# Optimization experiments

Measured on AMD Instinct MI355X. Metric: run time of the kernel, lower is better.

## Reference

```python
import jax, jax.numpy as jnp
import numpy as np

HIDDEN = 1024
HEADS = 16
HEAD_DIM = HIDDEN // HEADS          # 64
ROT = 2 * (HEAD_DIM // 3 // 2)      # 20 (d/h/w rotary chunk), residual = 4
GRID = 256 // 16                    # crop_size // patch_size = 16
DEPTH = 16 // 2                     # frames_per_clip // tubelet_size = 8
N_VIDEO = DEPTH * GRID * GRID       # 2048
N_ACTION = 16
B = 2
SCALE = HEAD_DIM ** -0.5


def _rope(x, pos):
    # interleaved RoPE (VJEPA2 rotate_queries_or_keys): pairs (x[2i], x[2i+1])
    D = x.shape[-1]
    omega = 1.0 / (10000.0 ** (jnp.arange(D // 2, dtype=x.dtype) / (D / 2.0)))
    freq = pos.astype(x.dtype)[..., None] * omega          # (N, D/2)
    cos, sin = jnp.cos(freq), jnp.sin(freq)
    x1, x2 = x[..., 0::2], x[..., 1::2]
    return jnp.stack([x1 * cos - x2 * sin, x2 * cos + x1 * sin], axis=-1).reshape(x.shape)


def _rope3(qk, d_pos, h_pos, w_pos):
    # rotate three ROT-sized chunks (depth/height/width axes), leave residual dims as-is
    parts = [_rope(qk[..., 0:ROT], d_pos),
             _rope(qk[..., ROT:2 * ROT], h_pos),
             _rope(qk[..., 2 * ROT:3 * ROT], w_pos)]
    if 3 * ROT < HEAD_DIM:
        parts.append(qk[..., 3 * ROT:])
    return jnp.concatenate(parts, axis=-1)


def _forward(video_hidden_states, action_hidden_states, W_q, b_q, W_k, b_k, W_v, b_v,
             W_qa, b_qa, W_ka, b_ka, W_va, b_va, W_proj, b_proj, W_proj_a, b_proj_a):
    Bsz, Nv, _ = video_hidden_states.shape
    Na = action_hidden_states.shape[1]

    def proj(x, W, b):  # -> (B, H, N, Dh)
        y = x @ W.T + b
        return y.reshape(Bsz, -1, HEADS, HEAD_DIM).transpose(0, 2, 1, 3)

    qv = proj(video_hidden_states, W_q, b_q)
    kv = proj(video_hidden_states, W_k, b_k)
    vv = proj(video_hidden_states, W_v, b_v)

    # 3-axis position ids for raster-ordered video tokens
    ids = jnp.arange(Nv)
    tpf = GRID * GRID
    d_pos = ids // tpf
    rem = ids - tpf * d_pos
    h_pos = rem // GRID
    w_pos = rem - GRID * h_pos

    qv = _rope3(qv, d_pos, h_pos, w_pos)
    kv = _rope3(kv, d_pos, h_pos, w_pos)

    qa = proj(action_hidden_states, W_qa, b_qa)
    ka = proj(action_hidden_states, W_ka, b_ka)
    va = proj(action_hidden_states, W_va, b_va)

    # actions: linspace between frame-id of token 0 and token 1 (faithful to source)
    a_pos = jnp.linspace(d_pos[0].astype(jnp.float32), d_pos[1].astype(jnp.float32), Na)
    qa = _rope3(qa, a_pos, a_pos, a_pos)
    ka = _rope3(ka, a_pos, a_pos, a_pos)

    # joint attention over concatenated video+action token sequence
    q = jnp.concatenate([qv, qa], axis=2)
    k = jnp.concatenate([kv, ka], axis=2)
    v = jnp.concatenate([vv, va], axis=2)

    scores = jnp.einsum('bhqd,bhkd->bhqk', q, k) * SCALE
    probs = jax.nn.softmax(scores, axis=-1)
    ctx = jnp.einsum('bhqk,bhkd->bhqd', probs, v)
    ctx = ctx.transpose(0, 2, 1, 3).reshape(Bsz, Nv + Na, HIDDEN)

    out_video = ctx[:, :Nv] @ W_proj.T + b_proj
    out_action = ctx[:, Nv:] @ W_proj_a.T + b_proj_a
    return out_video, out_action


def setup_inputs() -> dict:
    key = jax.random.key(0)
    ks = jax.random.split(key, 12)
    sd = HIDDEN ** -0.5
    inp = {}
    for i, n in enumerate(['q', 'k', 'v', 'qa', 'ka', 'va', 'proj', 'proj_a']):
        inp[f'W_{n}'] = jax.random.normal(ks[i], (HIDDEN, HIDDEN), jnp.float32) * sd
        inp[f'b_{n}'] = jnp.zeros((HIDDEN,), jnp.float32)
    inp['video_hidden_states'] = jax.random.normal(ks[10], (B, N_VIDEO, HIDDEN), jnp.float32)
    inp['action_hidden_states'] = jax.random.normal(ks[11], (B, N_ACTION, HIDDEN), jnp.float32)
    return inp


def reference(video_hidden_states, action_hidden_states, W_q, b_q, W_k, b_k, W_v, b_v,
              W_qa, b_qa, W_ka, b_ka, W_va, b_va, W_proj, b_proj, W_proj_a, b_proj_a):
    return _forward(video_hidden_states, action_hidden_states, W_q, b_q, W_k, b_k, W_v, b_v,
                    W_qa, b_qa, W_ka, b_ka, W_va, b_va, W_proj, b_proj, W_proj_a, b_proj_a)
```

## Files before the change

kernel.cpp:

```cpp
#include <hip/hip_runtime.h>
#include <stdint.h>

#define HID   1024
#define NHEAD 16
#define HDIM  64
#define NV    2048
#define NA    16
#define NTOK  2064
#define BSZ   2
#define EXP_C1 0.18033688011112042f
#define EXP_C2 16.0f

typedef __bf16 bf16x8 __attribute__((ext_vector_type(8)));
typedef unsigned short u16x8 __attribute__((ext_vector_type(8)));
typedef unsigned short u16x4 __attribute__((ext_vector_type(4)));
typedef float f32x4 __attribute__((ext_vector_type(4)));

__device__ __forceinline__ unsigned short f2bf(float f) {
  unsigned u = __builtin_bit_cast(unsigned, f);
  u += 0x7FFFu + ((u >> 16) & 1u);
  return (unsigned short)(u >> 16);
}
__device__ __forceinline__ unsigned short f2bf_trunc(float f) {
  return (unsigned short)(__builtin_bit_cast(unsigned, f) >> 16);
}

__global__ __launch_bounds__(256) void qkv_kernel(
    const float* __restrict__ video, const float* __restrict__ action,
    const float* __restrict__ Wq, const float* __restrict__ bq,
    const float* __restrict__ Wk, const float* __restrict__ bk,
    const float* __restrict__ Wv, const float* __restrict__ bv,
    const float* __restrict__ Wqa, const float* __restrict__ bqa,
    const float* __restrict__ Wka, const float* __restrict__ bka,
    const float* __restrict__ Wva, const float* __restrict__ bva,
    unsigned short* __restrict__ Qo, unsigned short* __restrict__ Ko,
    unsigned short* __restrict__ Vt)
{
  __shared__ unsigned short As[64][40];
  __shared__ unsigned short Bs[64][40];

  const int tid  = threadIdx.x;
  const int wave = tid >> 6;
  const int lane = tid & 63;
  const int quad = lane >> 4;
  const int l16  = lane & 15;
  const int z    = blockIdx.z;
  const int y    = blockIdx.y;
  const int head = blockIdx.x;
  const int n0   = head * 64;

  int b, rows, tok0; const float* X; bool act;
  if (y < 64) { b = y >> 5; tok0 = (y & 31) * 64; rows = 64;
                X = video + ((size_t)b * NV + tok0) * HID; act = false; }
  else        { b = y - 64; tok0 = NV; rows = NA;
                X = action + (size_t)b * NA * HID; act = true; }

  const float* W; const float* bias; 
  if (z == 0)      { W = act ? Wqa : Wq; bias = act ? bqa : bq; }
  else if (z == 1) { W = act ? Wka : Wk; bias = act ? bka : bk; }
  else             { W = act ? Wva : Wv; bias = act ? bva : bv; }

  const int arow = tid >> 2;
  const int ac8  = (tid & 3) * 8;
  const int xr   = min(arow, rows - 1);

  f32x4 acc[4] = {};

  for (int kt = 0; kt < HID; kt += 32) {
    {
      const float* src = X + (size_t)xr * HID + kt + ac8;
      float4 f0 = *(const float4*)src;
      float4 f1 = *(const float4*)(src + 4);
      u16x8 v;
      v[0]=f2bf(f0.x); v[1]=f2bf(f0.y); v[2]=f2bf(f0.z); v[3]=f2bf(f0.w);
      v[4]=f2bf(f1.x); v[5]=f2bf(f1.y); v[6]=f2bf(f1.z); v[7]=f2bf(f1.w);
      *(u16x8*)&As[arow][ac8] = v;
    }
    {
      const float* src = W + (size_t)(n0 + arow) * HID + kt + ac8;
      float4 f0 = *(const float4*)src;
      float4 f1 = *(const float4*)(src + 4);
      u16x8 v;
      v[0]=f2bf(f0.x); v[1]=f2bf(f0.y); v[2]=f2bf(f0.z); v[3]=f2bf(f0.w);
      v[4]=f2bf(f1.x); v[5]=f2bf(f1.y); v[6]=f2bf(f1.z); v[7]=f2bf(f1.w);
      *(u16x8*)&Bs[arow][ac8] = v;
    }
    __syncthreads();
    bf16x8 a = __builtin_bit_cast(bf16x8, *(const u16x8*)&As[wave * 16 + l16][quad * 8]);
#pragma unroll
    for (int nt = 0; nt < 4; nt++) {
      bf16x8 bb = __builtin_bit_cast(bf16x8, *(const u16x8*)&Bs[nt * 16 + l16][quad * 8]);
      acc[nt] = __builtin_amdgcn_mfma_f32_16x16x32_bf16(a, bb, acc[nt], 0, 0, 0);
    }
    __syncthreads();
  }

  const int mbase = wave * 16 + quad * 4;

  if (z < 2) {
    unsigned short* O = (z == 0) ? Qo : Ko;
#pragma unroll
    for (int nt = 0; nt < 4; nt++) {
      const int col = nt * 16 + l16;
      float vals[4];
#pragma unroll
      for (int r = 0; r < 4; r++) vals[r] = acc[nt][r] + bias[n0 + col];
      if (!act && col < 60) {
        const int seg = (col >= 40) ? 2 : (col >= 20) ? 1 : 0;
        const int tin = col - seg * 20;
        const int jj  = tin >> 1;
        const bool evn = !(tin & 1);
        const float om = exp2f(-(float)jj * 1.3287712379549449f);
#pragma unroll
        for (int r = 0; r < 4; r++) {
          int tk = tok0 + mbase + r;
          int dp = tk >> 8, hp = (tk >> 4) & 15, wp = tk & 15;
          float pos = (seg == 0) ? (float)dp : (seg == 1) ? (float)hp : (float)wp;
          float fr = pos * om;
          float cs = cosf(fr), sn = sinf(fr);
          float part = __shfl_xor(vals[r], 1);
          vals[r] = evn ? (vals[r] * cs - part * sn) : (vals[r] * cs + part * sn);
        }
      }
#pragma unroll
      for (int r = 0; r < 4; r++) {
        int m = mbase + r;
        if (m < rows)
          O[(((size_t)b * NHEAD + head) * NTOK + tok0 + m) * HDIM + col] = f2bf(vals[r]);
      }
    }
  } else {
#pragma unroll
    for (int nt = 0; nt < 4; nt++) {
      const int col = nt * 16 + l16;
      u16x4 pk;
#pragma unroll
      for (int r = 0; r < 4; r++) pk[r] = f2bf(acc[nt][r] + bias[n0 + col]);
      if (mbase < rows)
        *(u16x4*)&Vt[(((size_t)b * NHEAD + head) * HDIM + col) * NTOK + tok0 + mbase] = pk;
    }
  }
}

__global__ __launch_bounds__(256) void attn_kernel(
    const unsigned short* __restrict__ Q,
    const unsigned short* __restrict__ K,
    const unsigned short* __restrict__ Vt,
    unsigned short* __restrict__ ctx)
{
  __shared__ unsigned short Qs[64][72];
  __shared__ unsigned short Ks[64][72];
  __shared__ unsigned short Vts[64][72];
  __shared__ unsigned short Ps[4][16][68];

  const int tid  = threadIdx.x;
  const int wave = tid >> 6;
  const int lane = tid & 63;
  const int quad = lane >> 4;
  const int l16  = lane & 15;
  const int bh   = blockIdx.y;
  const int q0   = blockIdx.x * 64;
  const unsigned short* Qp  = Q  + (size_t)bh * NTOK * HDIM;
  const unsigned short* Kp  = K  + (size_t)bh * NTOK * HDIM;
  const unsigned short* Vtp = Vt + (size_t)bh * HDIM * NTOK;

  const int r  = tid >> 2;
  const int c0 = (tid & 3) * 8;

  {
    int row = min(q0 + r, NTOK - 1);
#pragma unroll
    for (int cc = 0; cc < 2; cc++) {
      int c = c0 + cc * 32;
      *(u16x8*)&Qs[r][c] = *(const u16x8*)(Qp + (size_t)row * HDIM + c);
    }
  }

  u16x8 ones_u;
#pragma unroll
  for (int i = 0; i < 8; i++) ones_u[i] = 0x3F80;
  const bf16x8 ones = __builtin_bit_cast(bf16x8, ones_u);

  f32x4 oacc[4] = {};
  f32x4 lacc = {};

  for (int kv0 = 0; kv0 < NTOK; kv0 += 64) {
    __syncthreads();
    {
      int row = min(kv0 + r, NTOK - 1);
#pragma unroll
      for (int cc = 0; cc < 2; cc++) {
        int c = c0 + cc * 32;
        *(u16x8*)&Ks[r][c]  = *(const u16x8*)(Kp + (size_t)row * HDIM + c);
        *(u16x8*)&Vts[r][c] = *(const u16x8*)(Vtp + (size_t)r * NTOK + kv0 + c);
      }
    }
    __syncthreads();

    f32x4 sacc[4] = {};
#pragma unroll
    for (int kq = 0; kq < 64; kq += 32) {
      bf16x8 a = __builtin_bit_cast(bf16x8, *(const u16x8*)&Qs[wave * 16 + l16][kq + quad * 8]);
#pragma unroll
      for (int nt = 0; nt < 4; nt++) {
        bf16x8 bb = __builtin_bit_cast(bf16x8, *(const u16x8*)&Ks[nt * 16 + l16][kq + quad * 8]);
        sacc[nt] = __builtin_amdgcn_mfma_f32_16x16x32_bf16(a, bb, sacc[nt], 0, 0, 0);
      }
    }

#pragma unroll
    for (int nt = 0; nt < 4; nt++) {
      bool valid = (kv0 + nt * 16 + l16) < NTOK;
#pragma unroll
      for (int rr = 0; rr < 4; rr++) {
        float p = exp2f(__builtin_fmaf(sacc[nt][rr], EXP_C1, -EXP_C2));
        p = valid ? p : 0.f;
        Ps[wave][quad * 4 + rr][nt * 16 + l16] = f2bf_trunc(p);
      }
    }

#pragma unroll
    for (int kq = 0; kq < 64; kq += 32) {
      u16x4 alo = *(const u16x4*)&Ps[wave][l16][kq + quad * 8];
      u16x4 ahi = *(const u16x4*)&Ps[wave][l16][kq + quad * 8 + 4];
      bf16x8 a = __builtin_bit_cast(bf16x8,
          __builtin_shufflevector(alo, ahi, 0, 1, 2, 3, 4, 5, 6, 7));
#pragma unroll
      for (int nt = 0; nt < 4; nt++) {
        bf16x8 bb = __builtin_bit_cast(bf16x8, *(const u16x8*)&Vts[nt * 16 + l16][kq + quad * 8]);
        oacc[nt] = __builtin_amdgcn_mfma_f32_16x16x32_bf16(a, bb, oacc[nt], 0, 0, 0);
      }
      lacc = __builtin_amdgcn_mfma_f32_16x16x32_bf16(a, ones, lacc, 0, 0, 0);
    }
  }

  const int b = bh >> 4, h = bh & 15;
  float rl[4];
#pragma unroll
  for (int rr = 0; rr < 4; rr++) rl[rr] = 1.f / lacc[rr];
#pragma unroll
  for (int nt = 0; nt < 4; nt++) {
#pragma unroll
    for (int rr = 0; rr < 4; rr++) {
      int token = q0 + wave * 16 + quad * 4 + rr;
      if (token < NTOK) {
        int d = nt * 16 + l16;
        ctx[((size_t)b * NTOK + token) * HID + h * HDIM + d] = f2bf(oacc[nt][rr] * rl[rr]);
      }
    }
  }
}

__global__ __launch_bounds__(256) void proj_kernel(
    const unsigned short* __restrict__ ctx,
    const float* __restrict__ Wp, const float* __restrict__ bp,
    const float* __restrict__ Wpa, const float* __restrict__ bpa,
    float* __restrict__ out)
{
  __shared__ unsigned short As[64][40];
  __shared__ unsigned short Bs[64][40];

  const int tid  = threadIdx.x;
  const int wave = tid >> 6;
  const int lane = tid & 63;
  const int quad = lane >> 4;
  const int l16  = lane & 15;
  const int y    = blockIdx.y;
  const int n0   = blockIdx.x * 64;

  int b, rows, tok0; bool act;
  if (y < 64) { b = y >> 5; tok0 = (y & 31) * 64; rows = 64; act = false; }
  else        { b = y - 64; tok0 = NV; rows = NA; act = true; }

  const unsigned short* X = ctx + ((size_t)b * NTOK + tok0) * HID;
  const float* W = act ? Wpa : Wp;
  const float* bias = act ? bpa : bp;

  const int arow = tid >> 2;
  const int ac8  = (tid & 3) * 8;
  const int xr   = min(arow, rows - 1);

  f32x4 acc[4] = {};

  for (int kt = 0; kt < HID; kt += 32) {
    *(u16x8*)&As[arow][ac8] = *(const u16x8*)(X + (size_t)xr * HID + kt + ac8);
    {
      const float* src = W + (size_t)(n0 + arow) * HID + kt + ac8;
      float4 f0 = *(const float4*)src;
      float4 f1 = *(const float4*)(src + 4);
      u16x8 v;
      v[0]=f2bf(f0.x); v[1]=f2bf(f0.y); v[2]=f2bf(f0.z); v[3]=f2bf(f0.w);
      v[4]=f2bf(f1.x); v[5]=f2bf(f1.y); v[6]=f2bf(f1.z); v[7]=f2bf(f1.w);
      *(u16x8*)&Bs[arow][ac8] = v;
    }
    __syncthreads();
    bf16x8 a = __builtin_bit_cast(bf16x8, *(const u16x8*)&As[wave * 16 + l16][quad * 8]);
#pragma unroll
    for (int nt = 0; nt < 4; nt++) {
      bf16x8 bb = __builtin_bit_cast(bf16x8, *(const u16x8*)&Bs[nt * 16 + l16][quad * 8]);
      acc[nt] = __builtin_amdgcn_mfma_f32_16x16x32_bf16(a, bb, acc[nt], 0, 0, 0);
    }
    __syncthreads();
  }

#pragma unroll
  for (int nt = 0; nt < 4; nt++) {
#pragma unroll
    for (int r = 0; r < 4; r++) {
      int m = wave * 16 + quad * 4 + r;
      if (m < rows) {
        int colg = n0 + nt * 16 + l16;
        float val = acc[nt][r] + bias[colg];
        if (!act)
          out[((size_t)b * NV + tok0 + m) * HID + colg] = val;
        else
          out[(size_t)BSZ * NV * HID + ((size_t)b * NA + m) * HID + colg] = val;
      }
    }
  }
}

extern "C" void kernel_launch(void* const* d_in, const int* in_sizes, int n_in,
                              void* d_out, int out_size, void* d_ws, size_t ws_size,
                              hipStream_t stream) {
  const float* A[18];
  if (in_sizes[0] == HID * HID) {
    for (int i = 0; i < 18; i++) A[i] = (const float*)d_in[i];
  } else {
    A[16] = (const float*)d_in[0];
    A[17] = (const float*)d_in[1];
    for (int i = 0; i < 16; i++) A[i] = (const float*)d_in[i + 2];
  }
  const float *Wq = A[0], *bq = A[1], *Wk = A[2], *bk = A[3], *Wv = A[4], *bv = A[5];
  const float *Wqa = A[6], *bqa = A[7], *Wka = A[8], *bka = A[9], *Wva = A[10], *bva = A[11];
  const float *Wp = A[12], *bp = A[13], *Wpa = A[14], *bpa = A[15];
  const float *video = A[16], *action = A[17];
  float* out = (float*)d_out;

  const size_t qkv_elems = (size_t)BSZ * NHEAD * NTOK * HDIM;
  unsigned short* Qw  = (unsigned short*)d_ws;
  unsigned short* Kw  = Qw + qkv_elems;
  unsigned short* Vtw = Kw + qkv_elems;
  unsigned short* ctx = Vtw + qkv_elems;

  dim3 g1(16, 66, 3);
  qkv_kernel<<<g1, 256, 0, stream>>>(video, action, Wq, bq, Wk, bk, Wv, bv,
                                     Wqa, bqa, Wka, bka, Wva, bva, Qw, Kw, Vtw);
  dim3 g3(33, BSZ * NHEAD);
  attn_kernel<<<g3, 256, 0, stream>>>(Qw, Kw, Vtw, ctx);
  dim3 g4(16, 66);
  proj_kernel<<<g4, 256, 0, stream>>>(ctx, Wp, bp, Wpa, bpa, out);
}
```

Baseline: 371.5 us.

## Pre-convert inputs to bf16 and use 128x128 async-LDS GEMM tiles for projections

Adds a conversion kernel that turns all weights and activations into bf16 once, instead of converting fp32 inside every GEMM tile load. The QKV and output projection GEMMs move from 64x64 to 128x128 tiles, with each wave computing a 4x4 grid of MFMA tiles, and load tiles with global_load_lds direct-to-LDS copies. Video and action rows are flattened into one M dimension, which changes the ctx layout. In exchange there is an extra launch plus workspace traffic, the LDS tiles are unpadded so bank conflicts are possible, and the larger tiles yield fewer blocks.

```diff
diff --git a/kernel.cpp b/kernel.cpp
--- a/kernel.cpp
+++ b/kernel.cpp
@@ -8,6 +8,8 @@
 #define NA    16
 #define NTOK  2064
 #define BSZ   2
+#define MROWS 4128
+#define WSZ   1048576
 #define EXP_C1 0.18033688011112042f
 #define EXP_C2 16.0f
 
@@ -24,120 +26,155 @@
 __device__ __forceinline__ unsigned short f2bf_trunc(float f) {
   return (unsigned short)(__builtin_bit_cast(unsigned, f) >> 16);
 }
-
-__global__ __launch_bounds__(256) void qkv_kernel(
+__device__ __forceinline__ void async_copy16(const void* g, void* l) {
+  __builtin_amdgcn_global_load_lds(
+      (const __attribute__((address_space(1))) unsigned int*)g,
+      (__attribute__((address_space(3))) unsigned int*)l, 16, 0, 0);
+}
+
+__global__ __launch_bounds__(256) void cvt_kernel(
+    const float* __restrict__ W0, const float* __restrict__ W1,
+    const float* __restrict__ W2, const float* __restrict__ W3,
+    const float* __restrict__ W4, const float* __restrict__ W5,
+    const float* __restrict__ W6, const float* __restrict__ W7,
     const float* __restrict__ video, const float* __restrict__ action,
-    const float* __restrict__ Wq, const float* __restrict__ bq,
-    const float* __restrict__ Wk, const float* __restrict__ bk,
-    const float* __restrict__ Wv, const float* __restrict__ bv,
-    const float* __restrict__ Wqa, const float* __restrict__ bqa,
-    const float* __restrict__ Wka, const float* __restrict__ bka,
-    const float* __restrict__ Wva, const float* __restrict__ bva,
+    unsigned short* __restrict__ Wb, unsigned short* __restrict__ Xb)
+{
+  const int y = blockIdx.y;
+  const size_t idx = ((size_t)blockIdx.x * 256 + threadIdx.x) * 8;
+  const float* src; unsigned short* dst;
+  if      (y == 0)  { src = W0; dst = Wb; }
+  else if (y == 1)  { src = W1; dst = Wb + 1 * WSZ; }
+  else if (y == 2)  { src = W2; dst = Wb + 2 * WSZ; }
+  else if (y == 3)  { src = W3; dst = Wb + 3 * WSZ; }
+  else if (y == 4)  { src = W4; dst = Wb + 4 * WSZ; }
+  else if (y == 5)  { src = W5; dst = Wb + 5 * WSZ; }
+  else if (y == 6)  { src = W6; dst = Wb + 6 * WSZ; }
+  else if (y == 7)  { src = W7; dst = Wb + 7 * WSZ; }
+  else if (y < 12)  { src = video + (size_t)(y - 8) * WSZ; dst = Xb + (size_t)(y - 8) * WSZ; }
+  else              { if (idx >= (size_t)BSZ * NA * HID) return;
+                      src = action; dst = Xb + (size_t)4096 * HID; }
+  float4 f0 = *(const float4*)(src + idx);
+  float4 f1 = *(const float4*)(src + idx + 4);
+  u16x8 v;
+  v[0]=f2bf(f0.x); v[1]=f2bf(f0.y); v[2]=f2bf(f0.z); v[3]=f2bf(f0.w);
+  v[4]=f2bf(f1.x); v[5]=f2bf(f1.y); v[6]=f2bf(f1.z); v[7]=f2bf(f1.w);
+  *(u16x8*)(dst + idx) = v;
+}
+
+__device__ __forceinline__ void row2bt(int rg, int& b, int& tok, bool& valid) {
+  if (rg < 4096) { b = rg >> 11; tok = rg & 2047; valid = true; }
+  else { int t = rg - 4096; b = t >> 4; tok = 2048 + (t & 15); valid = rg < MROWS; }
+}
+
+__global__ __launch_bounds__(256) void qkv128_kernel(
+    const unsigned short* __restrict__ Xb, const unsigned short* __restrict__ Wb,
+    const float* __restrict__ bq, const float* __restrict__ bk,
+    const float* __restrict__ bv, const float* __restrict__ bqa,
+    const float* __restrict__ bka, const float* __restrict__ bva,
     unsigned short* __restrict__ Qo, unsigned short* __restrict__ Ko,
     unsigned short* __restrict__ Vt)
 {
-  __shared__ unsigned short As[64][40];
-  __shared__ unsigned short Bs[64][40];
+  __shared__ unsigned short As[128 * 32];
+  __shared__ unsigned short Bs[128 * 32];
 
   const int tid  = threadIdx.x;
-  const int wave = tid >> 6;
-  const int lane = tid & 63;
-  const int quad = lane >> 4;
-  const int l16  = lane & 15;
+  const int w    = tid >> 6;
+  const int l    = tid & 63;
+  const int quad = l >> 4;
+  const int l16  = l & 15;
+  const int lrow = l >> 2;
+  const int lk   = (l & 3) * 8;
   const int z    = blockIdx.z;
-  const int y    = blockIdx.y;
-  const int head = blockIdx.x;
-  const int n0   = head * 64;
-
-  int b, rows, tok0; const float* X; bool act;
-  if (y < 64) { b = y >> 5; tok0 = (y & 31) * 64; rows = 64;
-                X = video + ((size_t)b * NV + tok0) * HID; act = false; }
-  else        { b = y - 64; tok0 = NV; rows = NA;
-                X = action + (size_t)b * NA * HID; act = true; }
-
-  const float* W; const float* bias; 
-  if (z == 0)      { W = act ? Wqa : Wq; bias = act ? bqa : bq; }
-  else if (z == 1) { W = act ? Wka : Wk; bias = act ? bka : bk; }
-  else             { W = act ? Wva : Wv; bias = act ? bva : bv; }
-
-  const int arow = tid >> 2;
-  const int ac8  = (tid & 3) * 8;
-  const int xr   = min(arow, rows - 1);
-
-  f32x4 acc[4] = {};
+  const int m0   = blockIdx.y * 128;
+  const int n0   = blockIdx.x * 128;
+  const bool atile = (blockIdx.y == 32);
+
+  const unsigned short* Wm = Wb + (size_t)(atile ? 3 + z : z) * WSZ;
+  const float* bias = (z == 0) ? (atile ? bqa : bq)
+                    : (z == 1) ? (atile ? bka : bk)
+                               : (atile ? bva : bv);
+
+  const int am = (w & 1) * 64;
+  const int bn = (w >> 1) * 64;
+
+  f32x4 acc[4][4] = {};
 
   for (int kt = 0; kt < HID; kt += 32) {
-    {
-      const float* src = X + (size_t)xr * HID + kt + ac8;
-      float4 f0 = *(const float4*)src;
-      float4 f1 = *(const float4*)(src + 4);
-      u16x8 v;
-      v[0]=f2bf(f0.x); v[1]=f2bf(f0.y); v[2]=f2bf(f0.z); v[3]=f2bf(f0.w);
-      v[4]=f2bf(f1.x); v[5]=f2bf(f1.y); v[6]=f2bf(f1.z); v[7]=f2bf(f1.w);
-      *(u16x8*)&As[arow][ac8] = v;
-    }
-    {
-      const float* src = W + (size_t)(n0 + arow) * HID + kt + ac8;
-      float4 f0 = *(const float4*)src;
-      float4 f1 = *(const float4*)(src + 4);
-      u16x8 v;
-      v[0]=f2bf(f0.x); v[1]=f2bf(f0.y); v[2]=f2bf(f0.z); v[3]=f2bf(f0.w);
-      v[4]=f2bf(f1.x); v[5]=f2bf(f1.y); v[6]=f2bf(f1.z); v[7]=f2bf(f1.w);
-      *(u16x8*)&Bs[arow][ac8] = v;
-    }
-    __syncthreads();
-    bf16x8 a = __builtin_bit_cast(bf16x8, *(const u16x8*)&As[wave * 16 + l16][quad * 8]);
-#pragma unroll
-    for (int nt = 0; nt < 4; nt++) {
-      bf16x8 bb = __builtin_bit_cast(bf16x8, *(const u16x8*)&Bs[nt * 16 + l16][quad * 8]);
-      acc[nt] = __builtin_amdgcn_mfma_f32_16x16x32_bf16(a, bb, acc[nt], 0, 0, 0);
-    }
-    __syncthreads();
-  }
-
-  const int mbase = wave * 16 + quad * 4;
+    __syncthreads();
+#pragma unroll
+    for (int i = 0; i < 2; i++) {
+      int trow = w * 32 + i * 16;
+      int arow = min(m0 + trow + lrow, MROWS - 1);
+      async_copy16(Xb + (size_t)arow * HID + kt + lk, &As[trow * 32]);
+      async_copy16(Wm + (size_t)(n0 + trow + lrow) * HID + kt + lk, &Bs[trow * 32]);
+    }
+    __syncthreads();
+
+    bf16x8 af[4], bf[4];
+#pragma unroll
+    for (int mi = 0; mi < 4; mi++)
+      af[mi] = __builtin_bit_cast(bf16x8, *(const u16x8*)&As[(am + mi * 16 + l16) * 32 + quad * 8]);
+#pragma unroll
+    for (int ni = 0; ni < 4; ni++)
+      bf[ni] = __builtin_bit_cast(bf16x8, *(const u16x8*)&Bs[(bn + ni * 16 + l16) * 32 + quad * 8]);
+#pragma unroll
+    for (int mi = 0; mi < 4; mi++)
+#pragma unroll
+      for (int ni = 0; ni < 4; ni++)
+        acc[mi][ni] = __builtin_amdgcn_mfma_f32_16x16x32_bf16(af[mi], bf[ni], acc[mi][ni], 0, 0, 0);
+  }
 
   if (z < 2) {
     unsigned short* O = (z == 0) ? Qo : Ko;
 #pragma unroll
-    for (int nt = 0; nt < 4; nt++) {
-      const int col = nt * 16 + l16;
-      float vals[4];
-#pragma unroll
-      for (int r = 0; r < 4; r++) vals[r] = acc[nt][r] + bias[n0 + col];
-      if (!act && col < 60) {
+    for (int mi = 0; mi < 4; mi++) {
+      const int rgb = m0 + am + mi * 16 + quad * 4;
+#pragma unroll
+      for (int ni = 0; ni < 4; ni++) {
+        const int gcol = n0 + bn + ni * 16 + l16;
+        const int head = gcol >> 6, col = gcol & 63;
+        const float bias_v = bias[gcol];
         const int seg = (col >= 40) ? 2 : (col >= 20) ? 1 : 0;
         const int tin = col - seg * 20;
-        const int jj  = tin >> 1;
+        const float om = exp2f(-(float)(tin >> 1) * 1.3287712379549449f);
         const bool evn = !(tin & 1);
-        const float om = exp2f(-(float)jj * 1.3287712379549449f);
 #pragma unroll
         for (int r = 0; r < 4; r++) {
-          int tk = tok0 + mbase + r;
-          int dp = tk >> 8, hp = (tk >> 4) & 15, wp = tk & 15;
-          float pos = (seg == 0) ? (float)dp : (seg == 1) ? (float)hp : (float)wp;
-          float fr = pos * om;
-          float cs = cosf(fr), sn = sinf(fr);
-          float part = __shfl_xor(vals[r], 1);
-          vals[r] = evn ? (vals[r] * cs - part * sn) : (vals[r] * cs + part * sn);
+          int rg = rgb + r;
+          int b, tok; bool valid;
+          row2bt(rg, b, tok, valid);
+          float val = acc[mi][ni][r] + bias_v;
+          float part = __shfl_xor(val, 1);
+          if (tok < 2048 && col < 60) {
+            int dp = tok >> 8, hp = (tok >> 4) & 15, wp = tok & 15;
+            float pos = (seg == 0) ? (float)dp : (seg == 1) ? (float)hp : (float)wp;
+            float fr = pos * om;
+            float cs = cosf(fr), sn = sinf(fr);
+            val = evn ? (val * cs - part * sn) : (val * cs + part * sn);
+          }
+          if (valid)
+            O[(((size_t)b * NHEAD + head) * NTOK + tok) * HDIM + col] = f2bf(val);
         }
       }
-#pragma unroll
-      for (int r = 0; r < 4; r++) {
-        int m = mbase + r;
-        if (m < rows)
-          O[(((size_t)b * NHEAD + head) * NTOK + tok0 + m) * HDIM + col] = f2bf(vals[r]);
-      }
     }
   } else {
 #pragma unroll
-    for (int nt = 0; nt < 4; nt++) {
-      const int col = nt * 16 + l16;
-      u16x4 pk;
-#pragma unroll
-      for (int r = 0; r < 4; r++) pk[r] = f2bf(acc[nt][r] + bias[n0 + col]);
-      if (mbase < rows)
-        *(u16x4*)&Vt[(((size_t)b * NHEAD + head) * HDIM + col) * NTOK + tok0 + mbase] = pk;
+    for (int mi = 0; mi < 4; mi++) {
+      const int rgb = m0 + am + mi * 16 + quad * 4;
+      int b, tok; bool valid;
+      row2bt(rgb, b, tok, valid);
+#pragma unroll
+      for (int ni = 0; ni < 4; ni++) {
+        const int gcol = n0 + bn + ni * 16 + l16;
+        const int head = gcol >> 6, d = gcol & 63;
+        const float bias_v = bias[gcol];
+        u16x4 pk;
+#pragma unroll
+        for (int r = 0; r < 4; r++) pk[r] = f2bf(acc[mi][ni][r] + bias_v);
+        if (valid)
+          *(u16x4*)&Vt[(((size_t)b * NHEAD + head) * HDIM + d) * NTOK + tok] = pk;
+      }
     }
   }
 }
@@ -244,77 +281,77 @@
     for (int rr = 0; rr < 4; rr++) {
       int token = q0 + wave * 16 + quad * 4 + rr;
       if (token < NTOK) {
+        int row = (token < 2048) ? (b * 2048 + token) : (4096 + b * NA + (token - 2048));
         int d = nt * 16 + l16;
-        ctx[((size_t)b * NTOK + token) * HID + h * HDIM + d] = f2bf(oacc[nt][rr] * rl[rr]);
-      }
-    }
-  }
-}
-
-__global__ __launch_bounds__(256) void proj_kernel(
-    const unsigned short* __restrict__ ctx,
-    const float* __restrict__ Wp, const float* __restrict__ bp,
-    const float* __restrict__ Wpa, const float* __restrict__ bpa,
+        ctx[(size_t)row * HID + h * HDIM + d] = f2bf(oacc[nt][rr] * rl[rr]);
+      }
+    }
+  }
+}
+
+__global__ __launch_bounds__(256) void proj128_kernel(
+    const unsigned short* __restrict__ ctx, const unsigned short* __restrict__ Wb,
+    const float* __restrict__ bp, const float* __restrict__ bpa,
     float* __restrict__ out)
 {
-  __shared__ unsigned short As[64][40];
-  __shared__ unsigned short Bs[64][40];
+  __shared__ unsigned short As[128 * 32];
+  __shared__ unsigned short Bs[128 * 32];
 
   const int tid  = threadIdx.x;
-  const int wave = tid >> 6;
-  const int lane = tid & 63;
-  const int quad = lane >> 4;
-  const int l16  = lane & 15;
-  const int y    = blockIdx.y;
-  const int n0   = blockIdx.x * 64;
-
-  int b, rows, tok0; bool act;
-  if (y < 64) { b = y >> 5; tok0 = (y & 31) * 64; rows = 64; act = false; }
-  else        { b = y - 64; tok0 = NV; rows = NA; act = true; }
-
-  const unsigned short* X = ctx + ((size_t)b * NTOK + tok0) * HID;
-  const float* W = act ? Wpa : Wp;
-  const float* bias = act ? bpa : bp;
-
-  const int arow = tid >> 2;
-  const int ac8  = (tid & 3) * 8;
-  const int xr   = min(arow, rows - 1);
-
-  f32x4 acc[4] = {};
+  const int w    = tid >> 6;
+  const int l    = tid & 63;
+  const int quad = l >> 4;
+  const int l16  = l & 15;
+  const int lrow = l >> 2;
+  const int lk   = (l & 3) * 8;
+  const int m0   = blockIdx.y * 128;
+  const int n0   = blockIdx.x * 128;
+  const bool atile = (blockIdx.y == 32);
+
+  const unsigned short* Wm = Wb + (size_t)(atile ? 7 : 6) * WSZ;
+  const float* bias = atile ? bpa : bp;
+
+  const int am = (w & 1) * 64;
+  const int bn = (w >> 1) * 64;
+
+  f32x4 acc[4][4] = {};
 
   for (int kt = 0; kt < HID; kt += 32) {
-    *(u16x8*)&As[arow][ac8] = *(const u16x8*)(X + (size_t)xr * HID + kt + ac8);
-    {
-      const float* src = W + (size_t)(n0 + arow) * HID + kt + ac8;
-      float4 f0 = *(const float4*)src;
-      float4 f1 = *(const float4*)(src + 4);
-      u16x8 v;
-      v[0]=f2bf(f0.x); v[1]=f2bf(f0.y); v[2]=f2bf(f0.z); v[3]=f2bf(f0.w);
-      v[4]=f2bf(f1.x); v[5]=f2bf(f1.y); v[6]=f2bf(f1.z); v[7]=f2bf(f1.w);
-      *(u16x8*)&Bs[arow][ac8] = v;
-    }
-    __syncthreads();
-    bf16x8 a = __builtin_bit_cast(bf16x8, *(const u16x8*)&As[wave * 16 + l16][quad * 8]);
-#pragma unroll
-    for (int nt = 0; nt < 4; nt++) {
-      bf16x8 bb = __builtin_bit_cast(bf16x8, *(const u16x8*)&Bs[nt * 16 + l16][quad * 8]);
-      acc[nt] = __builtin_amdgcn_mfma_f32_16x16x32_bf16(a, bb, acc[nt], 0, 0, 0);
-    }
-    __syncthreads();
-  }
-
-#pragma unroll
-  for (int nt = 0; nt < 4; nt++) {
-#pragma unroll
-    for (int r = 0; r < 4; r++) {
-      int m = wave * 16 + quad * 4 + r;
-      if (m < rows) {
-        int colg = n0 + nt * 16 + l16;
-        float val = acc[nt][r] + bias[colg];
-        if (!act)
-          out[((size_t)b * NV + tok0 + m) * HID + colg] = val;
-        else
-          out[(size_t)BSZ * NV * HID + ((size_t)b * NA + m) * HID + colg] = val;
+    __syncthreads();
+#pragma unroll
+    for (int i = 0; i < 2; i++) {
+      int trow = w * 32 + i * 16;
+      int arow = min(m0 + trow + lrow, MROWS - 1);
+      async_copy16(ctx + (size_t)arow * HID + kt + lk, &As[trow * 32]);
+      async_copy16(Wm + (size_t)(n0 + trow + lrow) * HID + kt + lk, &Bs[trow * 32]);
+    }
+    __syncthreads();
+
+    bf16x8 af[4], bf[4];
+#pragma unroll
+    for (int mi = 0; mi < 4; mi++)
+      af[mi] = __builtin_bit_cast(bf16x8, *(const u16x8*)&As[(am + mi * 16 + l16) * 32 + quad * 8]);
+#pragma unroll
+    for (int ni = 0; ni < 4; ni++)
+      bf[ni] = __builtin_bit_cast(bf16x8, *(const u16x8*)&Bs[(bn + ni * 16 + l16) * 32 + quad * 8]);
+#pragma unroll
+    for (int mi = 0; mi < 4; mi++)
+#pragma unroll
+      for (int ni = 0; ni < 4; ni++)
+        acc[mi][ni] = __builtin_amdgcn_mfma_f32_16x16x32_bf16(af[mi], bf[ni], acc[mi][ni], 0, 0, 0);
+  }
+
+#pragma unroll
+  for (int mi = 0; mi < 4; mi++) {
+    const int rgb = m0 + am + mi * 16 + quad * 4;
+#pragma unroll
+    for (int ni = 0; ni < 4; ni++) {
+      const int gcol = n0 + bn + ni * 16 + l16;
+      const float bias_v = bias[gcol];
+#pragma unroll
+      for (int r = 0; r < 4; r++) {
+        int rg = rgb + r;
+        if (rg < MROWS) out[(size_t)rg * HID + gcol] = acc[mi][ni][r] + bias_v;
       }
     }
   }
@@ -338,16 +375,21 @@
   float* out = (float*)d_out;
 
   const size_t qkv_elems = (size_t)BSZ * NHEAD * NTOK * HDIM;
-  unsigned short* Qw  = (unsigned short*)d_ws;
+  unsigned short* Wb  = (unsigned short*)d_ws;
+  unsigned short* Xb  = Wb + (size_t)8 * WSZ;
+  unsigned short* Qw  = Xb + (size_t)MROWS * HID;
   unsigned short* Kw  = Qw + qkv_elems;
   unsigned short* Vtw = Kw + qkv_elems;
   unsigned short* ctx = Vtw + qkv_elems;
 
-  dim3 g1(16, 66, 3);
-  qkv_kernel<<<g1, 256, 0, stream>>>(video, action, Wq, bq, Wk, bk, Wv, bv,
-                                     Wqa, bqa, Wka, bka, Wva, bva, Qw, Kw, Vtw);
-  dim3 g3(33, BSZ * NHEAD);
-  attn_kernel<<<g3, 256, 0, stream>>>(Qw, Kw, Vtw, ctx);
-  dim3 g4(16, 66);
-  proj_kernel<<<g4, 256, 0, stream>>>(ctx, Wp, bp, Wpa, bpa, out);
-}
+  dim3 g0(512, 13);
+  cvt_kernel<<<g0, 256, 0, stream>>>(Wq, Wk, Wv, Wqa, Wka, Wva, Wp, Wpa,
+                                     video, action, Wb, Xb);
+  dim3 g1(8, 33, 3);
+  qkv128_kernel<<<g1, 256, 0, stream>>>(Xb, Wb, bq, bk, bv, bqa, bka, bva,
+                                        Qw, Kw, Vtw);
+  dim3 g2(33, BSZ * NHEAD);
+  attn_kernel<<<g2, 256, 0, stream>>>(Qw, Kw, Vtw, ctx);
+  dim3 g3(8, 33);
+  proj128_kernel<<<g3, 256, 0, stream>>>(ctx, Wb, bp, bpa, out);
+}
```

Measured after the change: 382.1 us. +2.9%, slower.
